# Kernel tuning notes

Hardware: AMD Instinct MI355X
Metric: run time of the kernel (lower is better)

## Reference

```python
import jax, jax.numpy as jnp
import numpy as np

WS = 10      # window_size
HID = 32     # hidden_dim
B, T = 1024, 4096


def setup_inputs() -> dict:
    key = jax.random.key(0)
    k = jax.random.split(key, 7)
    returns = jax.random.normal(k[0], (B, T), dtype=jnp.float32) * 0.01
    W1 = jax.random.normal(k[1], (WS, HID), dtype=jnp.float32) * (1.0 / np.sqrt(WS))
    b1 = jnp.zeros((HID,), dtype=jnp.float32)
    W2 = jax.random.normal(k[2], (HID, HID), dtype=jnp.float32) * (1.0 / np.sqrt(HID))
    b2 = jnp.zeros((HID,), dtype=jnp.float32)
    W3 = jax.random.normal(k[3], (HID, 1), dtype=jnp.float32) * (1.0 / np.sqrt(HID))
    b3 = jnp.zeros((1,), dtype=jnp.float32)
    return {"returns": returns, "W1": W1, "b1": b1, "W2": W2, "b2": b2, "W3": W3, "b3": b3}


def reference(returns, W1, b1, W2, b2, W3, b3):
    ws = W1.shape[0]
    Bb, Tt = returns.shape
    # Unfold all sliding windows at once: windows[b, i, :] = returns[b, i:i+ws]
    # (window ending just before timestep t = i + ws)
    idx = jnp.arange(Tt - ws)[:, None] + jnp.arange(ws)[None, :]  # [T-ws, ws]
    windows = returns[:, idx]                                     # [B, T-ws, ws]
    h = jax.nn.relu(windows @ W1 + b1)                            # [B, T-ws, HID]
    h = jax.nn.relu(h @ W2 + b2)                                  # [B, T-ws, HID]
    out = 0.5 * jax.nn.sigmoid((h @ W3 + b3).squeeze(-1))         # [B, T-ws]
    # H_local[:, t] = out[:, t-ws] for t >= ws; first ws columns copy column ws
    head = jnp.broadcast_to(out[:, :1], (Bb, ws))                 # [B, ws]
    return jnp.concatenate([head, out], axis=1)                   # [B, T]
```

## Files before the change

### kernel.cpp

```cpp
#include <hip/hip_runtime.h>
#include <math.h>

typedef _Float16 f16x8  __attribute__((ext_vector_type(8)));
typedef _Float16 h2v    __attribute__((ext_vector_type(2)));
typedef float    f32x16 __attribute__((ext_vector_type(16)));
typedef float    f32x4  __attribute__((ext_vector_type(4)));
typedef __fp16   h2a    __attribute__((ext_vector_type(2)));
typedef unsigned u32x4  __attribute__((ext_vector_type(4)));

#define WS    10
#define HID   32
#define BDIM  256
#define NWAVE 4
#define GN    32
#define T_LEN 4096
#define NGRP  (T_LEN / GN)
#define PADN  4104

__device__ inline unsigned pack2u(float a, float b) {
    h2a t = __builtin_amdgcn_cvt_pkrtz(a, b);
    return __builtin_bit_cast(unsigned, t);
}
__device__ inline unsigned relu2(unsigned u) {
    h2v x = __builtin_bit_cast(h2v, u);
    h2v z = {(_Float16)0.0f, (_Float16)0.0f};
    return __builtin_bit_cast(unsigned, __builtin_elementwise_max(x, z));
}

__global__ __launch_bounds__(BDIM, 4)
void hurst_ldsrow(const float* __restrict__ returns,
                  const float* __restrict__ W1, const float* __restrict__ b1,
                  const float* __restrict__ W2, const float* __restrict__ b2,
                  const float* __restrict__ W3, const float* __restrict__ b3,
                  float* __restrict__ out)
{
    __shared__ __align__(16) _Float16 sbuf[2 * PADN];

    const int tid  = threadIdx.x;
    const int wid  = tid >> 6;
    const int lane = tid & 63;
    const int n    = lane & 31;
    const int hi   = lane >> 5;

    f32x16 b1v, b2v;
    #pragma unroll
    for (int i = 0; i < 4; ++i) {
        const f32x4 v1 = ((const f32x4*)b1)[2 * i + hi];
        const f32x4 v2 = ((const f32x4*)b2)[2 * i + hi];
        #pragma unroll
        for (int o = 0; o < 4; ++o) {
            b1v[4 * i + o] = v1[o];
            b2v[4 * i + o] = v2[o];
        }
    }
    const float corr = b3[0] - b2[4 * hi];

    f16x8 a1, a2lo, a2hi, a3lo, a3hi;
    #pragma unroll
    for (int jj = 0; jj < 8; ++jj) {
        const int k  = 8 * hi + jj;
        a1[jj] = (k < WS) ? (_Float16)W1[k * HID + n] : (_Float16)0.0f;
        const int kf = (k & 3) | ((k & 4) << 1) | ((k & 8) >> 1);
        a2lo[jj] = (_Float16)W2[kf * HID + n];
        a2hi[jj] = (_Float16)W2[(16 + kf) * HID + n];
        a3lo[jj] = (_Float16)W3[kf];
        a3hi[jj] = (_Float16)W3[16 + kf];
    }

    const float* rp   = returns + (size_t)blockIdx.x * T_LEN;
    float*       optr = out     + (size_t)blockIdx.x * T_LEN;

    {
        float f[17];
        __builtin_memcpy(f, rp + 16 * tid, 64);
        const int nx = 16 * tid + 16;
        f[16] = rp[(nx < T_LEN) ? nx : (T_LEN - 1)];

        u32x4 q0a, q0b, q1a, q1b;
        #pragma unroll
        for (int k = 0; k < 4; ++k) {
            q0a[k] = pack2u(f[2 * k],     f[2 * k + 1]);
            q0b[k] = pack2u(f[8 + 2 * k], f[9 + 2 * k]);
            q1a[k] = pack2u(f[2 * k + 1], f[2 * k + 2]);
            q1b[k] = pack2u(f[9 + 2 * k], f[10 + 2 * k]);
        }
        unsigned* s32 = (unsigned*)sbuf;
        *(u32x4*)(s32 + 8 * tid)                  = q0a;
        *(u32x4*)(s32 + 8 * tid + 4)              = q0b;
        *(u32x4*)(s32 + (PADN / 2) + 8 * tid)     = q1a;
        *(u32x4*)(s32 + (PADN / 2) + 8 * tid + 4) = q1b;
    }
    __syncthreads();

    for (int g = wid; g < NGRP; g += NWAVE) {
        const int tg = g * GN + n;
        const int ws = (tg >= WS) ? (tg - WS) : 0;

        const unsigned eoff = (ws & 1) ? (unsigned)(PADN + ws - 1) : (unsigned)ws;
        u32x4 q;
        __builtin_memcpy(&q, (const char*)sbuf + 2 * eoff + 8 * hi, 16);
        u32x4 xu;
        xu[0] = hi ? q[2] : q[0];
        xu[1] = hi ? 0u   : q[1];
        xu[2] = hi ? 0u   : q[2];
        xu[3] = hi ? 0u   : q[3];
        const f16x8 xb = __builtin_bit_cast(f16x8, xu);

        f32x16 d1 = __builtin_amdgcn_mfma_f32_32x32x16_f16(a1, xb, b1v, 0, 0, 0);

        u32x4 p1lo, p1hi;
        #pragma unroll
        for (int qq = 0; qq < 4; ++qq) {
            p1lo[qq] = relu2(pack2u(d1[2 * qq],     d1[2 * qq + 1]));
            p1hi[qq] = relu2(pack2u(d1[8 + 2 * qq], d1[9 + 2 * qq]));
        }

        f32x16 d2 = __builtin_amdgcn_mfma_f32_32x32x16_f16(
                        a2lo, __builtin_bit_cast(f16x8, p1lo), b2v, 0, 0, 0);
        d2 = __builtin_amdgcn_mfma_f32_32x32x16_f16(
                        a2hi, __builtin_bit_cast(f16x8, p1hi), d2, 0, 0, 0);

        u32x4 p2lo, p2hi;
        #pragma unroll
        for (int qq = 0; qq < 4; ++qq) {
            p2lo[qq] = relu2(pack2u(d2[2 * qq],     d2[2 * qq + 1]));
            p2hi[qq] = relu2(pack2u(d2[8 + 2 * qq], d2[9 + 2 * qq]));
        }

        f32x16 d3 = __builtin_amdgcn_mfma_f32_32x32x16_f16(
                        a3lo, __builtin_bit_cast(f16x8, p2lo), b2v, 0, 0, 0);
        d3 = __builtin_amdgcn_mfma_f32_32x32x16_f16(
                        a3hi, __builtin_bit_cast(f16x8, p2hi), d3, 0, 0, 0);

        const float o = 0.5f * __builtin_amdgcn_rcpf(1.0f + __expf(-(d3[0] + corr)));
        if (hi == 0)
            optr[tg] = o;
    }
}

extern "C" void kernel_launch(void* const* d_in, const int* in_sizes, int n_in,
                              void* d_out, int out_size, void* d_ws, size_t ws_size,
                              hipStream_t stream) {
    const float* returns = (const float*)d_in[0];
    const float* W1      = (const float*)d_in[1];
    const float* b1      = (const float*)d_in[2];
    const float* W2      = (const float*)d_in[3];
    const float* b2      = (const float*)d_in[4];
    const float* W3      = (const float*)d_in[5];
    const float* b3      = (const float*)d_in[6];
    float* out = (float*)d_out;

    const int B = out_size / T_LEN;

    dim3 grid(B, 1, 1);
    dim3 block(BDIM, 1, 1);
    hurst_ldsrow<<<grid, block, 0, stream>>>(returns, W1, b1, W2, b2, W3, b3, out);
}
```

Measured before the change: 99.55 us.

## Switch MLP MFMAs from 32x32x16 to 16x16x32 tiles with 16-timestep groups

Rebuilds the per-wave MLP evaluation around 16x16x32 f16 MFMA instructions instead of 32x32x16. Each wave now processes 16 timesteps per iteration instead of 32. Hidden units are split into two 16-wide halves, with a new permutation mapping the weights into the new operand layout. The third layer now folds b3 directly into its accumulator, removing the old bias correction term. The aim is shorter dependent MFMA latency and fewer registers per step. The cost is twice as many loop iterations, so per-group LDS reads, sigmoid work and stores are doubled, and each store now uses only 16 lanes.

```diff
diff --git a/kernel.cpp b/kernel.cpp
--- a/kernel.cpp
+++ b/kernel.cpp
@@ -1,18 +1,17 @@
 #include <hip/hip_runtime.h>
 #include <math.h>
 
-typedef _Float16 f16x8  __attribute__((ext_vector_type(8)));
-typedef _Float16 h2v    __attribute__((ext_vector_type(2)));
-typedef float    f32x16 __attribute__((ext_vector_type(16)));
-typedef float    f32x4  __attribute__((ext_vector_type(4)));
-typedef __fp16   h2a    __attribute__((ext_vector_type(2)));
-typedef unsigned u32x4  __attribute__((ext_vector_type(4)));
+typedef _Float16 f16x8 __attribute__((ext_vector_type(8)));
+typedef _Float16 h2v   __attribute__((ext_vector_type(2)));
+typedef float    f32x4 __attribute__((ext_vector_type(4)));
+typedef __fp16   h2a   __attribute__((ext_vector_type(2)));
+typedef unsigned u32x4 __attribute__((ext_vector_type(4)));
 
 #define WS    10
 #define HID   32
 #define BDIM  256
 #define NWAVE 4
-#define GN    32
+#define GN    16
 #define T_LEN 4096
 #define NGRP  (T_LEN / GN)
 #define PADN  4104
@@ -27,8 +26,13 @@
     return __builtin_bit_cast(unsigned, __builtin_elementwise_max(x, z));
 }
 
+__device__ inline int sigma(int j) {
+    const int q = j >> 3, u = j & 7;
+    return (u < 4) ? (4 * q + u) : (16 + 4 * q + (u - 4));
+}
+
 __global__ __launch_bounds__(BDIM, 4)
-void hurst_ldsrow(const float* __restrict__ returns,
+void hurst_mfma16(const float* __restrict__ returns,
                   const float* __restrict__ W1, const float* __restrict__ b1,
                   const float* __restrict__ W2, const float* __restrict__ b2,
                   const float* __restrict__ W3, const float* __restrict__ b3,
@@ -39,32 +43,29 @@
     const int tid  = threadIdx.x;
     const int wid  = tid >> 6;
     const int lane = tid & 63;
-    const int n    = lane & 31;
-    const int hi   = lane >> 5;
+    const int c    = lane & 15;
+    const int q    = lane >> 4;
 
-    f32x16 b1v, b2v;
+    f32x4 b1va, b1vb, b2va, b2vb, b3v;
     #pragma unroll
-    for (int i = 0; i < 4; ++i) {
-        const f32x4 v1 = ((const f32x4*)b1)[2 * i + hi];
-        const f32x4 v2 = ((const f32x4*)b2)[2 * i + hi];
-        #pragma unroll
-        for (int o = 0; o < 4; ++o) {
-            b1v[4 * i + o] = v1[o];
-            b2v[4 * i + o] = v2[o];
-        }
+    for (int r = 0; r < 4; ++r) {
+        b1va[r] = b1[4 * q + r];
+        b1vb[r] = b1[16 + 4 * q + r];
+        b2va[r] = b2[4 * q + r];
+        b2vb[r] = b2[16 + 4 * q + r];
+        b3v[r]  = b3[0];
     }
-    const float corr = b3[0] - b2[4 * hi];
 
-    f16x8 a1, a2lo, a2hi, a3lo, a3hi;
+    f16x8 a1a, a1b, a2a, a2b, a3;
     #pragma unroll
     for (int jj = 0; jj < 8; ++jj) {
-        const int k  = 8 * hi + jj;
-        a1[jj] = (k < WS) ? (_Float16)W1[k * HID + n] : (_Float16)0.0f;
-        const int kf = (k & 3) | ((k & 4) << 1) | ((k & 8) >> 1);
-        a2lo[jj] = (_Float16)W2[kf * HID + n];
-        a2hi[jj] = (_Float16)W2[(16 + kf) * HID + n];
-        a3lo[jj] = (_Float16)W3[kf];
-        a3hi[jj] = (_Float16)W3[16 + kf];
+        const int k = 8 * q + jj;
+        a1a[jj] = (k < WS) ? (_Float16)W1[k * HID + c]        : (_Float16)0.0f;
+        a1b[jj] = (k < WS) ? (_Float16)W1[k * HID + 16 + c]   : (_Float16)0.0f;
+        const int s = sigma(k);
+        a2a[jj] = (_Float16)W2[s * HID + c];
+        a2b[jj] = (_Float16)W2[s * HID + 16 + c];
+        a3[jj]  = (_Float16)W3[s];
     }
 
     const float* rp   = returns + (size_t)blockIdx.x * T_LEN;
@@ -75,7 +76,6 @@
         __builtin_memcpy(f, rp + 16 * tid, 64);
         const int nx = 16 * tid + 16;
         f[16] = rp[(nx < T_LEN) ? nx : (T_LEN - 1)];
-
         u32x4 q0a, q0b, q1a, q1b;
         #pragma unroll
         for (int k = 0; k < 4; ++k) {
@@ -93,47 +93,43 @@
     __syncthreads();
 
     for (int g = wid; g < NGRP; g += NWAVE) {
-        const int tg = g * GN + n;
+        const int tg = g * GN + c;
         const int ws = (tg >= WS) ? (tg - WS) : 0;
 
         const unsigned eoff = (ws & 1) ? (unsigned)(PADN + ws - 1) : (unsigned)ws;
-        u32x4 q;
-        __builtin_memcpy(&q, (const char*)sbuf + 2 * eoff + 8 * hi, 16);
+        u32x4 qv;
+        __builtin_memcpy(&qv, (const char*)sbuf + 2 * (eoff + ((q == 1) ? 8u : 0u)), 16);
         u32x4 xu;
-        xu[0] = hi ? q[2] : q[0];
-        xu[1] = hi ? 0u   : q[1];
-        xu[2] = hi ? 0u   : q[2];
-        xu[3] = hi ? 0u   : q[3];
+        xu[0] = (q < 2) ? qv[0] : 0u;
+        xu[1] = (q == 0) ? qv[1] : 0u;
+        xu[2] = (q == 0) ? qv[2] : 0u;
+        xu[3] = (q == 0) ? qv[3] : 0u;
         const f16x8 xb = __builtin_bit_cast(f16x8, xu);
 
-        f32x16 d1 = __builtin_amdgcn_mfma_f32_32x32x16_f16(a1, xb, b1v, 0, 0, 0);
+        const f32x4 d1a = __builtin_amdgcn_mfma_f32_16x16x32_f16(a1a, xb, b1va, 0, 0, 0);
+        const f32x4 d1b = __builtin_amdgcn_mfma_f32_16x16x32_f16(a1b, xb, b1vb, 0, 0, 0);
 
-        u32x4 p1lo, p1hi;
-        #pragma unroll
-        for (int qq = 0; qq < 4; ++qq) {
-            p1lo[qq] = relu2(pack2u(d1[2 * qq],     d1[2 * qq + 1]));
-            p1hi[qq] = relu2(pack2u(d1[8 + 2 * qq], d1[9 + 2 * qq]));
-        }
+        u32x4 p1;
+        p1[0] = relu2(pack2u(d1a[0], d1a[1]));
+        p1[1] = relu2(pack2u(d1a[2], d1a[3]));
+        p1[2] = relu2(pack2u(d1b[0], d1b[1]));
+        p1[3] = relu2(pack2u(d1b[2], d1b[3]));
+        const f16x8 h1 = __builtin_bit_cast(f16x8, p1);
 
-        f32x16 d2 = __builtin_amdgcn_mfma_f32_32x32x16_f16(
-                        a2lo, __builtin_bit_cast(f16x8, p1lo), b2v, 0, 0, 0);
-        d2 = __builtin_amdgcn_mfma_f32_32x32x16_f16(
-                        a2hi, __builtin_bit_cast(f16x8, p1hi), d2, 0, 0, 0);
+        const f32x4 d2a = __builtin_amdgcn_mfma_f32_16x16x32_f16(a2a, h1, b2va, 0, 0, 0);
+        const f32x4 d2b = __builtin_amdgcn_mfma_f32_16x16x32_f16(a2b, h1, b2vb, 0, 0, 0);
 
-        u32x4 p2lo, p2hi;
-        #pragma unroll
-        for (int qq = 0; qq < 4; ++qq) {
-            p2lo[qq] = relu2(pack2u(d2[2 * qq],     d2[2 * qq + 1]));
-            p2hi[qq] = relu2(pack2u(d2[8 + 2 * qq], d2[9 + 2 * qq]));
-        }
+        u32x4 p2;
+        p2[0] = relu2(pack2u(d2a[0], d2a[1]));
+        p2[1] = relu2(pack2u(d2a[2], d2a[3]));
+        p2[2] = relu2(pack2u(d2b[0], d2b[1]));
+        p2[3] = relu2(pack2u(d2b[2], d2b[3]));
+        const f16x8 h2 = __builtin_bit_cast(f16x8, p2);
 
-        f32x16 d3 = __builtin_amdgcn_mfma_f32_32x32x16_f16(
-                        a3lo, __builtin_bit_cast(f16x8, p2lo), b2v, 0, 0, 0);
-        d3 = __builtin_amdgcn_mfma_f32_32x32x16_f16(
-                        a3hi, __builtin_bit_cast(f16x8, p2hi), d3, 0, 0, 0);
+        const f32x4 d3 = __builtin_amdgcn_mfma_f32_16x16x32_f16(a3, h2, b3v, 0, 0, 0);
 
-        const float o = 0.5f * __builtin_amdgcn_rcpf(1.0f + __expf(-(d3[0] + corr)));
-        if (hi == 0)
+        const float o = 0.5f * __builtin_amdgcn_rcpf(1.0f + __expf(-d3[0]));
+        if (q == 0)
             optr[tg] = o;
     }
 }
@@ -154,5 +150,5 @@
 
     dim3 grid(B, 1, 1);
     dim3 block(BDIM, 1, 1);
-    hurst_ldsrow<<<grid, block, 0, stream>>>(returns, W1, b1, W2, b2, W3, b3, out);
+    hurst_mfma16<<<grid, block, 0, stream>>>(returns, W1, b1, W2, b2, W3, b3, out);
 }
```

After: 111.3 us. +11.8%, slower.
